# Performance work log

Hardware: AMD Instinct MI355X
Metric: run time of the kernel (lower is better)

The kernel has to match this reference:

```python
import jax, jax.numpy as jnp
import numpy as np

E = 1024
M = 6
GH = 256
FR = 16  # FiLM bottleneck r = max(16, E//64)


def setup_inputs() -> dict:
    key = jax.random.key(0)
    ks = jax.random.split(key, 32)
    n = lambda k, shape, std=0.02: jax.random.normal(k, shape, dtype=jnp.float32) * std
    inp = {
        "x": jax.random.normal(ks[0], (4, 2048, E), dtype=jnp.float32),
        # gate MLP E->GH->M
        "gw1": n(ks[1], (E, GH)), "gb1": jnp.zeros((GH,), jnp.float32),
        "gw2": n(ks[2], (GH, M)), "gb2": jnp.zeros((M,), jnp.float32),
        "ebias": jnp.zeros((M,), jnp.float32),
        "pm_alpha": jnp.float32(0.5),
        # expert 0: DoubleMLP E->2E->E
        "dfc_w": n(ks[3], (E, 2 * E)), "dfc_b": jnp.zeros((2 * E,), jnp.float32),
        "dproj_w": n(ks[4], (2 * E, E)), "dproj_b": jnp.zeros((E,), jnp.float32),
        # expert 1: SingleMLP E->E->E
        "sfc_w": n(ks[5], (E, E)), "sfc_b": jnp.zeros((E,), jnp.float32),
        "sproj_w": n(ks[6], (E, E)), "sproj_b": jnp.zeros((E,), jnp.float32),
        # expert 2: rank-2 perceptron
        "p2_w": n(ks[7], (2, E)), "p2_v": n(ks[8], (2, E)),
        "p2_alpha": jnp.ones((2,), jnp.float32), "p2_b": jnp.zeros((2,), jnp.float32),
        "p2_bias": jnp.zeros((E,), jnp.float32),
        # expert 3: rank-4 perceptron
        "p4_w": n(ks[9], (4, E)), "p4_v": n(ks[10], (4, E)),
        "p4_alpha": jnp.ones((4,), jnp.float32), "p4_b": jnp.zeros((4,), jnp.float32),
        "p4_bias": jnp.zeros((E,), jnp.float32),
        # expert 4: ReGLU1D
        "rg_u": n(ks[11], (E,)), "rg_a": jnp.ones((E,), jnp.float32),
        "rg_b": jnp.zeros((1,), jnp.float32), "rg_bias": jnp.zeros((E,), jnp.float32),
        # expert 5: FiLM E->FR->2E
        "fl_dw": n(ks[12], (E, FR)), "fl_db": jnp.zeros((FR,), jnp.float32),
        "fl_uw": n(ks[13], (FR, 2 * E)), "fl_ub": jnp.zeros((2 * E,), jnp.float32),
    }
    return inp


def _gelu(x):
    return jax.nn.gelu(x, approximate=False)  # torch nn.GELU default (erf)


def _rank_n(x, w, v, alpha, b, biasvec):
    # y = biasvec + sum_i alpha_i * gelu(<w_i,x> + b_i) * v_i
    s = jnp.einsum("bse,ne->bsn", x, w) + b
    g = _gelu(s)
    return jnp.einsum("bsn,ne->bse", alpha * g, v) + biasvec


def reference(x, gw1, gb1, gw2, gb2, ebias, pm_alpha,
              dfc_w, dfc_b, dproj_w, dproj_b,
              sfc_w, sfc_b, sproj_w, sproj_b,
              p2_w, p2_v, p2_alpha, p2_b, p2_bias,
              p4_w, p4_v, p4_alpha, p4_b, p4_bias,
              rg_u, rg_a, rg_b, rg_bias,
              fl_dw, fl_db, fl_uw, fl_ub):
    # gate logits [B,S,M]; tau=1.0
    gl = _gelu(x @ gw1 + gb1) @ gw2 + gb2 + ebias
    pi = jax.nn.softmax(gl, axis=-1)
    # top_k=1 sparse weights: mask to top-1 then renormalize
    _, topi = jax.lax.top_k(pi, 1)
    mask = jax.nn.one_hot(topi[..., 0], M, dtype=pi.dtype)
    w = pi * mask
    w = w / (jnp.sum(w, axis=-1, keepdims=True) + 1e-9)

    # experts (dropout = identity in eval)
    o0 = _gelu(x @ dfc_w + dfc_b) @ dproj_w + dproj_b            # DoubleMLP
    o1 = _gelu(x @ sfc_w + sfc_b) @ sproj_w + sproj_b            # SingleMLP
    o2 = _rank_n(x, p2_w, p2_v, p2_alpha, p2_b, p2_bias)          # perc2
    o3 = _rank_n(x, p4_w, p4_v, p4_alpha, p4_b, p4_bias)          # perc4
    s = x @ rg_u + rg_b[0]                                        # ReGLU1D
    o4 = jax.nn.sigmoid(s)[..., None] * (x * rg_a) + rg_bias
    t = _gelu(x @ fl_dw + fl_db)                                  # FiLM
    gb = t @ fl_uw + fl_ub
    gamma, beta = jnp.split(gb, 2, axis=-1)
    o5 = gamma * x + beta

    all_out = jnp.stack([o0, o1, o2, o3, o4, o5], axis=-1)        # [B,S,E,M]
    mixed = jnp.sum(all_out * w[..., None, :], axis=-1)
    return pm_alpha * mixed
```

## Files before the change

### kernel.cpp

```cpp
#include <hip/hip_runtime.h>
#include <math.h>


#define E 1024
#define GH 256
#define NEXP 6
#define NTOK 8192

typedef __attribute__((ext_vector_type(8))) short bf16x8;
typedef __attribute__((ext_vector_type(4))) float f32x4;

__device__ __forceinline__ float gelu_erf(float v) {
    return 0.5f * v * (1.0f + erff(v * 0.70710678118654752440f));
}

__device__ __forceinline__ unsigned short f2bf(float f) {
    union { float f; unsigned u; } c; c.f = f;
    unsigned u = c.u;
    u += 0x7fffu + ((u >> 16) & 1u);
    return (unsigned short)(u >> 16);
}

__device__ __forceinline__ float bf2f(unsigned short h) {
    union { unsigned u; float f; } c; c.u = ((unsigned)h) << 16;
    return c.f;
}

__device__ __forceinline__ float dot4(float4 a, float4 b) {
    return a.x * b.x + a.y * b.y + a.z * b.z + a.w * b.w;
}

__device__ __forceinline__ int ldso(int row, int q) {
    return row * 32 + ((q ^ ((row >> 1) & 3)) << 3);
}

__global__ __launch_bounds__(256)
void prep_kernel(const float* __restrict__ x, unsigned short* __restrict__ xh,
                 unsigned short* __restrict__ xl,
                 const float* __restrict__ gw1, unsigned short* __restrict__ w1cat,
                 const float* __restrict__ fl_dw, float* __restrict__ fl_dwT,
                 const float* __restrict__ dfc_w, unsigned short* __restrict__ dfc_wt,
                 const float* __restrict__ dproj_w, unsigned short* __restrict__ dpj_wt,
                 const float* __restrict__ sfc_w, unsigned short* __restrict__ sfc_wt,
                 const float* __restrict__ sproj_w, unsigned short* __restrict__ spj_wt) {
    __shared__ float tile[32][33];
    const int tid = threadIdx.x;
    const int tx = tid & 31, ty = tid >> 5;
    int b = blockIdx.x;
    if (b < 2048) {
        const int n4 = NTOK * E / 4;
        for (int i = b * 256 + tid; i < n4; i += 2048 * 256) {
            float4 v = reinterpret_cast<const float4*>(x)[i];
            ushort4 h, l;
            h.x = f2bf(v.x); l.x = f2bf(v.x - bf2f(h.x));
            h.y = f2bf(v.y); l.y = f2bf(v.y - bf2f(h.y));
            h.z = f2bf(v.z); l.z = f2bf(v.z - bf2f(h.z));
            h.w = f2bf(v.w); l.w = f2bf(v.w - bf2f(h.w));
            reinterpret_cast<ushort4*>(xh)[i] = h;
            reinterpret_cast<ushort4*>(xl)[i] = l;
        }
        return;
    }
    b -= 2048;
    if (b < 256) {
        const int c0 = (b & 7) * 32, r0 = (b >> 3) * 32;
#pragma unroll
        for (int i = 0; i < 4; ++i)
            tile[ty + i * 8][tx] = gw1[(size_t)(r0 + ty + i * 8) * GH + c0 + tx];
        __syncthreads();
#pragma unroll
        for (int i = 0; i < 4; ++i) {
            float v = tile[tx][ty + i * 8];
            unsigned short h = f2bf(v);
            size_t row = (size_t)(c0 + ty + i * 8) * 2048;
            w1cat[row + r0 + tx] = h;
            w1cat[row + 1024 + r0 + tx] = f2bf(v - bf2f(h));
        }
        return;
    }
    b -= 256;
    if (b < 64) {
        int idx = b * 256 + tid;
        int j = idx >> 10, k = idx & (E - 1);
        fl_dwT[idx] = fl_dw[k * 16 + j];
        return;
    }
    b -= 64;
    const float* src; unsigned short* dst; int R, C, nbx;
    if (b < 2048)      { src = dfc_w;   dst = dfc_wt; R = 1024; C = 2048; nbx = 64; }
    else if (b < 4096) { src = dproj_w; dst = dpj_wt; R = 2048; C = 1024; nbx = 32; b -= 2048; }
    else if (b < 5120) { src = sfc_w;   dst = sfc_wt; R = 1024; C = 1024; nbx = 32; b -= 4096; }
    else               { src = sproj_w; dst = spj_wt; R = 1024; C = 1024; nbx = 32; b -= 5120; }
    const int c0 = (b % nbx) * 32, r0 = (b / nbx) * 32;
#pragma unroll
    for (int i = 0; i < 4; ++i)
        tile[ty + i * 8][tx] = src[(size_t)(r0 + ty + i * 8) * C + c0 + tx];
    __syncthreads();
#pragma unroll
    for (int i = 0; i < 4; ++i)
        dst[(size_t)(c0 + ty + i * 8) * R + r0 + tx] = f2bf(tile[tx][ty + i * 8]);
}

__global__ __launch_bounds__(256)
void gate_partial_kernel(const unsigned short* __restrict__ xh,
                         const unsigned short* __restrict__ xl,
                         const unsigned short* __restrict__ w1cat,
                         float* __restrict__ hp0, float* __restrict__ hp1) {
    __shared__ __align__(16) unsigned short As[128 * 32];
    __shared__ __align__(16) unsigned short Bs[64 * 32];
    const int tid = threadIdx.x;
    const int t0 = blockIdx.y * 128, n0 = blockIdx.x * 64, z = blockIdx.z;
    const unsigned short* A = z ? xl : xh;
    float* hp = z ? hp1 : hp0;

    const int lane = tid & 63, wv = tid >> 6;
    const int wm = (wv & 1) * 64, wn = (wv >> 1) * 32;
    const int lm = lane & 15, q = lane >> 4;
    const int r0 = tid >> 2, gsl = tid & 3;
    const int g = gsl ^ ((r0 >> 1) & 3);

    const unsigned short* pa0 = A + (size_t)(t0 + r0) * E + g * 8;
    const unsigned short* pa1 = A + (size_t)(t0 + r0 + 64) * E + g * 8;
    const unsigned short* pb0 = w1cat + (size_t)(n0 + r0) * 2048 + g * 8;

    f32x4 acc[4][2];
#pragma unroll
    for (int s = 0; s < 4; ++s)
#pragma unroll
        for (int t = 0; t < 2; ++t) acc[s][t] = (f32x4){0.f, 0.f, 0.f, 0.f};

    bf16x8 ra0 = *(const bf16x8*)(pa0);
    bf16x8 ra1 = *(const bf16x8*)(pa1);
    bf16x8 rb0 = *(const bf16x8*)(pb0);
    *(bf16x8*)&As[r0 * 32 + gsl * 8] = ra0;
    *(bf16x8*)&As[(r0 + 64) * 32 + gsl * 8] = ra1;
    *(bf16x8*)&Bs[r0 * 32 + gsl * 8] = rb0;

    int k0 = 0;
    while (true) {
        __syncthreads();
        const int kn = k0 + 32;
        if (kn < 2048) {
            ra0 = *(const bf16x8*)(pa0 + (kn & 1023));
            ra1 = *(const bf16x8*)(pa1 + (kn & 1023));
            rb0 = *(const bf16x8*)(pb0 + kn);
        }
        bf16x8 af[4], bf[2];
#pragma unroll
        for (int s = 0; s < 4; ++s) af[s] = *(const bf16x8*)&As[ldso(wm + s * 16 + lm, q)];
#pragma unroll
        for (int t = 0; t < 2; ++t) bf[t] = *(const bf16x8*)&Bs[ldso(wn + t * 16 + lm, q)];
#pragma unroll
        for (int s = 0; s < 4; ++s)
#pragma unroll
            for (int t = 0; t < 2; ++t)
                acc[s][t] = __builtin_amdgcn_mfma_f32_16x16x32_bf16(af[s], bf[t], acc[s][t], 0, 0, 0);
        if (kn >= 2048) break;
        __syncthreads();
        *(bf16x8*)&As[r0 * 32 + gsl * 8] = ra0;
        *(bf16x8*)&As[(r0 + 64) * 32 + gsl * 8] = ra1;
        *(bf16x8*)&Bs[r0 * 32 + gsl * 8] = rb0;
        k0 = kn;
    }
#pragma unroll
    for (int s = 0; s < 4; ++s)
#pragma unroll
        for (int t = 0; t < 2; ++t)
#pragma unroll
            for (int rg = 0; rg < 4; ++rg) {
                int rl = wm + s * 16 + q * 4 + rg;
                int c  = wn + t * 16 + lm;
                hp[(size_t)(t0 + rl) * GH + n0 + c] = acc[s][t][rg];
            }
}

__global__ __launch_bounds__(256)
void gate_finalize_kernel(const float* __restrict__ hp0, const float* __restrict__ hp1,
                          const float* __restrict__ gb1, const float* __restrict__ gw2,
                          const float* __restrict__ gb2, const float* __restrict__ ebias,
                          const float* __restrict__ pm_alpha,
                          float* __restrict__ scale, int* __restrict__ counts,
                          int* __restrict__ tlist, int* __restrict__ eid) {
    __shared__ float hs[32][264];
    __shared__ float g2s[GH * NEXP];
    __shared__ int tokexp[32];
    const int tid = threadIdx.x;
    const int t0 = blockIdx.x * 32;
    for (int i = tid; i < GH * NEXP; i += 256) g2s[i] = gw2[i];
#pragma unroll
    for (int i = 0; i < 8; ++i) {
        int f4 = i * 256 + tid;
        int row = f4 >> 6, c4 = (f4 & 63) * 4;
        size_t base = (size_t)(t0 + row) * GH + c4;
        float4 a = *reinterpret_cast<const float4*>(&hp0[base]);
        float4 b = *reinterpret_cast<const float4*>(&hp1[base]);
        float4 o;
        o.x = gelu_erf(a.x + b.x + gb1[c4 + 0]);
        o.y = gelu_erf(a.y + b.y + gb1[c4 + 1]);
        o.z = gelu_erf(a.z + b.z + gb1[c4 + 2]);
        o.w = gelu_erf(a.w + b.w + gb1[c4 + 3]);
        *reinterpret_cast<float4*>(&hs[row][c4]) = o;
    }
    __syncthreads();
    const int t = tid >> 3, j = tid & 7;
    float p[NEXP] = {0.f, 0.f, 0.f, 0.f, 0.f, 0.f};
#pragma unroll 8
    for (int kk = 0; kk < 32; ++kk) {
        int k = j + kk * 8;
        float hv = hs[t][k];
        const float* gr = &g2s[k * NEXP];
#pragma unroll
        for (int m = 0; m < NEXP; ++m) p[m] += hv * gr[m];
    }
#pragma unroll
    for (int m = 0; m < NEXP; ++m) {
        p[m] += __shfl_xor(p[m], 4, 64);
        p[m] += __shfl_xor(p[m], 2, 64);
        p[m] += __shfl_xor(p[m], 1, 64);
    }
    if (j == 0) {
        float L[NEXP];
#pragma unroll
        for (int m = 0; m < NEXP; ++m) L[m] = p[m] + gb2[m] + ebias[m];
        float mx = L[0]; int am = 0;
#pragma unroll
        for (int m = 1; m < NEXP; ++m) { if (L[m] > mx) { mx = L[m]; am = m; } }
        float S = 0.f;
#pragma unroll
        for (int m = 0; m < NEXP; ++m) S += expf(L[m] - mx);
        float pt = 1.f / S;
        scale[t0 + t] = pm_alpha[0] * (pt / (pt + 1e-9f));
        eid[t0 + t] = am;
        tokexp[t] = am;
    }
    __syncthreads();
    if (tid < NEXP) {
        const int e = tid;
        int cnt = 0;
#pragma unroll
        for (int i = 0; i < 32; ++i) cnt += (tokexp[i] == e);
        if (cnt) {
            int base = atomicAdd(&counts[e], cnt);
            int pos = 0;
#pragma unroll
            for (int i = 0; i < 32; ++i)
                if (tokexp[i] == e) tlist[e * NTOK + base + (pos++)] = t0 + i;
        }
    }
}

__global__ __launch_bounds__(256)
void moe_gemm1_kernel(const unsigned short* __restrict__ xh,
                      const unsigned short* __restrict__ B0, const unsigned short* __restrict__ B1,
                      const float* __restrict__ bias0, const float* __restrict__ bias1,
                      const int* __restrict__ counts, const int* __restrict__ tlist,
                      unsigned short* __restrict__ H0, unsigned short* __restrict__ H1) {
    const int z = blockIdx.z;
    const int N = z ? 1024 : 2048;
    const int K = E;
    const int cnt = counts[z];
    const int i0 = blockIdx.y * 64;
    const int n0 = blockIdx.x * 64;
    if (i0 >= cnt || n0 >= N) return;
    const unsigned short* Bz = z ? B1 : B0;
    const float* bias = z ? bias1 : bias0;

    __shared__ __align__(16) unsigned short As[64 * 32];
    __shared__ __align__(16) unsigned short Bs[64 * 32];
    __shared__ int toks[64];
    const int tid = threadIdx.x;
    if (tid < 64) toks[tid] = tlist[z * NTOK + min(i0 + tid, cnt - 1)];
    __syncthreads();

    const int lane = tid & 63, wv = tid >> 6;
    const int wm = (wv & 1) * 32, wn = (wv >> 1) * 32;
    const int lm = lane & 15, q = lane >> 4;
    const int r0 = tid >> 2, gsl = tid & 3;
    const int g = gsl ^ ((r0 >> 1) & 3);

    const unsigned short* pa = xh + (size_t)toks[r0] * K + g * 8;
    const unsigned short* pb = Bz + (size_t)(n0 + r0) * K + g * 8;

    f32x4 acc[2][2];
#pragma unroll
    for (int s = 0; s < 2; ++s)
#pragma unroll
        for (int t = 0; t < 2; ++t) acc[s][t] = (f32x4){0.f, 0.f, 0.f, 0.f};

    bf16x8 ra = *(const bf16x8*)(pa);
    bf16x8 rb = *(const bf16x8*)(pb);
    *(bf16x8*)&As[r0 * 32 + gsl * 8] = ra;
    *(bf16x8*)&Bs[r0 * 32 + gsl * 8] = rb;

    int k0 = 0;
    while (true) {
        __syncthreads();
        const int kn = k0 + 32;
        if (kn < K) {
            ra = *(const bf16x8*)(pa + kn);
            rb = *(const bf16x8*)(pb + kn);
        }
        bf16x8 af[2], bf[2];
#pragma unroll
        for (int s = 0; s < 2; ++s) af[s] = *(const bf16x8*)&As[ldso(wm + s * 16 + lm, q)];
#pragma unroll
        for (int t = 0; t < 2; ++t) bf[t] = *(const bf16x8*)&Bs[ldso(wn + t * 16 + lm, q)];
#pragma unroll
        for (int s = 0; s < 2; ++s)
#pragma unroll
            for (int t = 0; t < 2; ++t)
                acc[s][t] = __builtin_amdgcn_mfma_f32_16x16x32_bf16(af[s], bf[t], acc[s][t], 0, 0, 0);
        if (kn >= K) break;
        __syncthreads();
        *(bf16x8*)&As[r0 * 32 + gsl * 8] = ra;
        *(bf16x8*)&Bs[r0 * 32 + gsl * 8] = rb;
        k0 = kn;
    }
    unsigned short* Hz = z ? H1 : H0;
#pragma unroll
    for (int s = 0; s < 2; ++s)
#pragma unroll
        for (int t = 0; t < 2; ++t)
#pragma unroll
            for (int rg = 0; rg < 4; ++rg) {
                int rl = wm + s * 16 + q * 4 + rg;
                int gc = n0 + wn + t * 16 + lm;
                float v = acc[s][t][rg] + bias[gc];
                Hz[(size_t)(i0 + rl) * N + gc] = f2bf(gelu_erf(v));
            }
}

__global__ __launch_bounds__(256)
void gemm2_cheap_kernel(const unsigned short* __restrict__ h1, const unsigned short* __restrict__ h2,
                        const unsigned short* __restrict__ dpj, const unsigned short* __restrict__ spj,
                        const float* __restrict__ dproj_b, const float* __restrict__ sproj_b,
                        const int* __restrict__ counts, const int* __restrict__ tlist,
                        const float* __restrict__ scale,
                        const float* __restrict__ x, const int* __restrict__ eid,
                        const float* __restrict__ p2_w, const float* __restrict__ p2_v,
                        const float* __restrict__ p2_alpha, const float* __restrict__ p2_b,
                        const float* __restrict__ p2_bias,
                        const float* __restrict__ p4_w, const float* __restrict__ p4_v,
                        const float* __restrict__ p4_alpha, const float* __restrict__ p4_b,
                        const float* __restrict__ p4_bias,
                        const float* __restrict__ rg_u, const float* __restrict__ rg_a,
                        const float* __restrict__ rg_b, const float* __restrict__ rg_bias,
                        const float* __restrict__ fl_dwT, const float* __restrict__ fl_db,
                        const float* __restrict__ fl_uw, const float* __restrict__ fl_ub,
                        float* __restrict__ out) {
    __shared__ __align__(16) char smem[64 * 32 * 2 * 2 + 64 * 4];
    const int tid = threadIdx.x;
    const int bb = blockIdx.x;

    if (bb < 1024) {
        const int z = bb >> 9;
        const int r = bb & 511;
        const int n0 = (r & 15) * 64;
        const int i0 = (r >> 4) * 64;
        const int K = z ? 1024 : 2048;
        const int cnt = counts[z];
        if (i0 >= cnt) return;
        const int rows = min(64, cnt - i0);
        const unsigned short* Az = z ? h2 : h1;
        const unsigned short* Bz = z ? spj : dpj;
        const float* bias = z ? sproj_b : dproj_b;

        unsigned short* As = (unsigned short*)smem;
        unsigned short* Bs = As + 64 * 32;
        int* toks = (int*)(Bs + 64 * 32);
        if (tid < 64) toks[tid] = tlist[z * NTOK + min(i0 + tid, cnt - 1)];
        __syncthreads();

        const int lane = tid & 63, wv = tid >> 6;
        const int wm = (wv & 1) * 32, wn = (wv >> 1) * 32;
        const int lm = lane & 15, q = lane >> 4;
        const int r0 = tid >> 2, gsl = tid & 3;
        const int g = gsl ^ ((r0 >> 1) & 3);

        const unsigned short* pa = Az + (size_t)(i0 + r0) * K + g * 8;
        const unsigned short* pb = Bz + (size_t)(n0 + r0) * K + g * 8;

        f32x4 acc[2][2];
#pragma unroll
        for (int s = 0; s < 2; ++s)
#pragma unroll
            for (int t = 0; t < 2; ++t) acc[s][t] = (f32x4){0.f, 0.f, 0.f, 0.f};

        bf16x8 ra = *(const bf16x8*)(pa);
        bf16x8 rb = *(const bf16x8*)(pb);
        *(bf16x8*)&As[r0 * 32 + gsl * 8] = ra;
        *(bf16x8*)&Bs[r0 * 32 + gsl * 8] = rb;

        int k0 = 0;
        while (true) {
            __syncthreads();
            const int kn = k0 + 32;
            if (kn < K) {
                ra = *(const bf16x8*)(pa + kn);
                rb = *(const bf16x8*)(pb + kn);
            }
            bf16x8 af[2], bf[2];
#pragma unroll
            for (int s = 0; s < 2; ++s) af[s] = *(const bf16x8*)&As[ldso(wm + s * 16 + lm, q)];
#pragma unroll
            for (int t = 0; t < 2; ++t) bf[t] = *(const bf16x8*)&Bs[ldso(wn + t * 16 + lm, q)];
#pragma unroll
            for (int s = 0; s < 2; ++s)
#pragma unroll
                for (int t = 0; t < 2; ++t)
                    acc[s][t] = __builtin_amdgcn_mfma_f32_16x16x32_bf16(af[s], bf[t], acc[s][t], 0, 0, 0);
            if (kn >= K) break;
            __syncthreads();
            *(bf16x8*)&As[r0 * 32 + gsl * 8] = ra;
            *(bf16x8*)&Bs[r0 * 32 + gsl * 8] = rb;
            k0 = kn;
        }
#pragma unroll
        for (int s = 0; s < 2; ++s)
#pragma unroll
            for (int t = 0; t < 2; ++t)
#pragma unroll
                for (int rg = 0; rg < 4; ++rg) {
                    int rl = wm + s * 16 + q * 4 + rg;
                    if (rl < rows) {
                        int gc = n0 + wn + t * 16 + lm;
                        int tok = toks[rl];
                        out[(size_t)tok * E + gc] = scale[tok] * (acc[s][t][rg] + bias[gc]);
                    }
                }
        return;
    }

    const int tok = bb - 1024;
    const int e = eid[tok];
    if (e < 2) return;
    float* red = (float*)smem;
    float* gs  = red + 64;
    const int k4 = tid * 4;
    const float4 xv = *reinterpret_cast<const float4*>(&x[(size_t)tok * E + k4]);
    const float sc = scale[tok];
    const int lane = tid & 63, wid = tid >> 6;
    float4 o;

    if (e == 2 || e == 3) {
        const int n = (e == 2) ? 2 : 4;
        const float* w    = (e == 2) ? p2_w : p4_w;
        const float* v    = (e == 2) ? p2_v : p4_v;
        const float* al   = (e == 2) ? p2_alpha : p4_alpha;
        const float* b    = (e == 2) ? p2_b : p4_b;
        const float* bias = (e == 2) ? p2_bias : p4_bias;
        for (int j = 0; j < n; ++j) {
            float val = dot4(xv, *reinterpret_cast<const float4*>(&w[j * E + k4]));
            for (int off = 32; off > 0; off >>= 1) val += __shfl_down(val, off, 64);
            if (lane == 0) red[j * 4 + wid] = val;
        }
        __syncthreads();
        if (tid < n) {
            float s = red[tid * 4] + red[tid * 4 + 1] + red[tid * 4 + 2] + red[tid * 4 + 3] + b[tid];
            gs[tid] = al[tid] * gelu_erf(s);
        }
        __syncthreads();
        o = *reinterpret_cast<const float4*>(&bias[k4]);
        for (int j = 0; j < n; ++j) {
            float4 vv = *reinterpret_cast<const float4*>(&v[j * E + k4]);
            float gj = gs[j];
            o.x += gj * vv.x; o.y += gj * vv.y; o.z += gj * vv.z; o.w += gj * vv.w;
        }
    } else if (e == 4) {
        float val = dot4(xv, *reinterpret_cast<const float4*>(&rg_u[k4]));
        for (int off = 32; off > 0; off >>= 1) val += __shfl_down(val, off, 64);
        if (lane == 0) red[wid] = val;
        __syncthreads();
        float s = red[0] + red[1] + red[2] + red[3] + rg_b[0];
        float sg = 1.f / (1.f + expf(-s));
        float4 av = *reinterpret_cast<const float4*>(&rg_a[k4]);
        float4 bv = *reinterpret_cast<const float4*>(&rg_bias[k4]);
        o.x = sg * xv.x * av.x + bv.x;
        o.y = sg * xv.y * av.y + bv.y;
        o.z = sg * xv.z * av.z + bv.z;
        o.w = sg * xv.w * av.w + bv.w;
    } else {
#pragma unroll
        for (int j = 0; j < 16; ++j) {
            float val = dot4(xv, *reinterpret_cast<const float4*>(&fl_dwT[j * E + k4]));
            for (int off = 32; off > 0; off >>= 1) val += __shfl_down(val, off, 64);
            if (lane == 0) red[j * 4 + wid] = val;
        }
        __syncthreads();
        if (tid < 16)
            gs[tid] = gelu_erf(red[tid * 4] + red[tid * 4 + 1] + red[tid * 4 + 2] + red[tid * 4 + 3] + fl_db[tid]);
        __syncthreads();
        float4 ga = *reinterpret_cast<const float4*>(&fl_ub[k4]);
        float4 be = *reinterpret_cast<const float4*>(&fl_ub[E + k4]);
#pragma unroll
        for (int j = 0; j < 16; ++j) {
            float tj = gs[j];
            float4 ug = *reinterpret_cast<const float4*>(&fl_uw[(size_t)j * 2 * E + k4]);
            float4 ub = *reinterpret_cast<const float4*>(&fl_uw[(size_t)j * 2 * E + E + k4]);
            ga.x += tj * ug.x; ga.y += tj * ug.y; ga.z += tj * ug.z; ga.w += tj * ug.w;
            be.x += tj * ub.x; be.y += tj * ub.y; be.z += tj * ub.z; be.w += tj * ub.w;
        }
        o.x = ga.x * xv.x + be.x;
        o.y = ga.y * xv.y + be.y;
        o.z = ga.z * xv.z + be.z;
        o.w = ga.w * xv.w + be.w;
    }
    o.x *= sc; o.y *= sc; o.z *= sc; o.w *= sc;
    *reinterpret_cast<float4*>(&out[(size_t)tok * E + k4]) = o;
}

extern "C" void kernel_launch(void* const* d_in, const int* in_sizes, int n_in,
                              void* d_out, int out_size, void* d_ws, size_t ws_size,
                              hipStream_t stream) {
    const float* x        = (const float*)d_in[0];
    const float* gw1      = (const float*)d_in[1];
    const float* gb1      = (const float*)d_in[2];
    const float* gw2      = (const float*)d_in[3];
    const float* gb2      = (const float*)d_in[4];
    const float* ebias    = (const float*)d_in[5];
    const float* pm_alpha = (const float*)d_in[6];
    const float* dfc_w    = (const float*)d_in[7];
    const float* dfc_b    = (const float*)d_in[8];
    const float* dproj_w  = (const float*)d_in[9];
    const float* dproj_b  = (const float*)d_in[10];
    const float* sfc_w    = (const float*)d_in[11];
    const float* sfc_b    = (const float*)d_in[12];
    const float* sproj_w  = (const float*)d_in[13];
    const float* sproj_b  = (const float*)d_in[14];
    const float* p2_w     = (const float*)d_in[15];
    const float* p2_v     = (const float*)d_in[16];
    const float* p2_alpha = (const float*)d_in[17];
    const float* p2_b     = (const float*)d_in[18];
    const float* p2_bias  = (const float*)d_in[19];
    const float* p4_w     = (const float*)d_in[20];
    const float* p4_v     = (const float*)d_in[21];
    const float* p4_alpha = (const float*)d_in[22];
    const float* p4_b     = (const float*)d_in[23];
    const float* p4_bias  = (const float*)d_in[24];
    const float* rg_u     = (const float*)d_in[25];
    const float* rg_a     = (const float*)d_in[26];
    const float* rg_b     = (const float*)d_in[27];
    const float* rg_bias  = (const float*)d_in[28];
    const float* fl_dw    = (const float*)d_in[29];
    const float* fl_db    = (const float*)d_in[30];
    const float* fl_uw    = (const float*)d_in[31];
    const float* fl_ub    = (const float*)d_in[32];
    float* out = (float*)d_out;

    char* ws = (char*)d_ws;
    size_t off = 0;
    int*            counts = (int*)(ws + off);            off += 256;
    float*          scale  = (float*)(ws + off);          off += (size_t)NTOK * 4;
    int*            tlist  = (int*)(ws + off);            off += (size_t)NEXP * NTOK * 4;
    int*            eid    = (int*)(ws + off);            off += (size_t)NTOK * 4;
    float*          fl_dwT = (float*)(ws + off);          off += (size_t)16 * E * 4;
    unsigned short* w1cat  = (unsigned short*)(ws + off); off += (size_t)GH * 2048 * 2;
    unsigned short* dfc_wt = (unsigned short*)(ws + off); off += (size_t)2048 * 1024 * 2;
    unsigned short* dpj_wt = (unsigned short*)(ws + off); off += (size_t)1024 * 2048 * 2;
    unsigned short* sfc_wt = (unsigned short*)(ws + off); off += (size_t)1024 * 1024 * 2;
    unsigned short* spj_wt = (unsigned short*)(ws + off); off += (size_t)1024 * 1024 * 2;
    unsigned short* x_hi   = (unsigned short*)(ws + off); off += (size_t)NTOK * E * 2;
    char* U = ws + off;
    unsigned short* x_lo = (unsigned short*)U;
    float*          hp0  = (float*)(U + (size_t)16 * 1024 * 1024);
    float*          hp1  = (float*)(U + (size_t)24 * 1024 * 1024);
    unsigned short* h1   = (unsigned short*)U;
    unsigned short* h2   = (unsigned short*)(U + (size_t)16 * 1024 * 1024);

    hipMemsetAsync(counts, 0, 256, stream);
    prep_kernel<<<8512, 256, 0, stream>>>(x, x_hi, x_lo, gw1, w1cat, fl_dw, fl_dwT,
                                          dfc_w, dfc_wt, dproj_w, dpj_wt,
                                          sfc_w, sfc_wt, sproj_w, spj_wt);
    gate_partial_kernel<<<dim3(GH / 64, NTOK / 128, 2), 256, 0, stream>>>(x_hi, x_lo, w1cat, hp0, hp1);
    gate_finalize_kernel<<<NTOK / 32, 256, 0, stream>>>(hp0, hp1, gb1, gw2, gb2, ebias,
                                                        pm_alpha, scale, counts, tlist, eid);
    moe_gemm1_kernel<<<dim3(32, 32, 2), 256, 0, stream>>>(
        x_hi, dfc_wt, sfc_wt, dfc_b, sfc_b, counts, tlist, h1, h2);
    gemm2_cheap_kernel<<<1024 + NTOK, 256, 0, stream>>>(
        h1, h2, dpj_wt, spj_wt, dproj_b, sproj_b, counts, tlist, scale,
        x, eid,
        p2_w, p2_v, p2_alpha, p2_b, p2_bias,
        p4_w, p4_v, p4_alpha, p4_b, p4_bias,
        rg_u, rg_a, rg_b, rg_bias,
        fl_dwT, fl_db, fl_uw, fl_ub, out);
    (void)in_sizes; (void)n_in; (void)out_size; (void)ws_size;
}
```

Measured before the change: 297.9 us.

## Double-buffer LDS tiles in all GEMM kernels and shrink gate tile to 64 rows

The three MFMA GEMM loops (gate partial, expert GEMM1, expert GEMM2) now keep two shared-memory buffers for A and B. Each k-step writes the next tile into the idle buffer, which removes one __syncthreads per iteration. The gate partial kernel also moves from 128-row to 64-row token tiles, doubling its grid to give more blocks and less per-block register use. In exchange, LDS usage per block doubles and the gate GEMM reloads weight tiles across twice as many blocks.

```diff
diff --git a/kernel.cpp b/kernel.cpp
--- a/kernel.cpp
+++ b/kernel.cpp
@@ -106,64 +106,59 @@
                          const unsigned short* __restrict__ xl,
                          const unsigned short* __restrict__ w1cat,
                          float* __restrict__ hp0, float* __restrict__ hp1) {
-    __shared__ __align__(16) unsigned short As[128 * 32];
-    __shared__ __align__(16) unsigned short Bs[64 * 32];
+    __shared__ __align__(16) unsigned short As[2][64 * 32];
+    __shared__ __align__(16) unsigned short Bs[2][64 * 32];
     const int tid = threadIdx.x;
-    const int t0 = blockIdx.y * 128, n0 = blockIdx.x * 64, z = blockIdx.z;
+    const int t0 = blockIdx.y * 64, n0 = blockIdx.x * 64, z = blockIdx.z;
     const unsigned short* A = z ? xl : xh;
     float* hp = z ? hp1 : hp0;
 
     const int lane = tid & 63, wv = tid >> 6;
-    const int wm = (wv & 1) * 64, wn = (wv >> 1) * 32;
+    const int wm = (wv & 1) * 32, wn = (wv >> 1) * 32;
     const int lm = lane & 15, q = lane >> 4;
     const int r0 = tid >> 2, gsl = tid & 3;
     const int g = gsl ^ ((r0 >> 1) & 3);
-
-    const unsigned short* pa0 = A + (size_t)(t0 + r0) * E + g * 8;
-    const unsigned short* pa1 = A + (size_t)(t0 + r0 + 64) * E + g * 8;
-    const unsigned short* pb0 = w1cat + (size_t)(n0 + r0) * 2048 + g * 8;
-
-    f32x4 acc[4][2];
-#pragma unroll
-    for (int s = 0; s < 4; ++s)
+    const int so = r0 * 32 + gsl * 8;
+
+    const unsigned short* pa = A + (size_t)(t0 + r0) * E + g * 8;
+    const unsigned short* pb = w1cat + (size_t)(n0 + r0) * 2048 + g * 8;
+
+    f32x4 acc[2][2];
+#pragma unroll
+    for (int s = 0; s < 2; ++s)
 #pragma unroll
         for (int t = 0; t < 2; ++t) acc[s][t] = (f32x4){0.f, 0.f, 0.f, 0.f};
 
-    bf16x8 ra0 = *(const bf16x8*)(pa0);
-    bf16x8 ra1 = *(const bf16x8*)(pa1);
-    bf16x8 rb0 = *(const bf16x8*)(pb0);
-    *(bf16x8*)&As[r0 * 32 + gsl * 8] = ra0;
-    *(bf16x8*)&As[(r0 + 64) * 32 + gsl * 8] = ra1;
-    *(bf16x8*)&Bs[r0 * 32 + gsl * 8] = rb0;
-
-    int k0 = 0;
+    bf16x8 ra = *(const bf16x8*)(pa);
+    bf16x8 rb = *(const bf16x8*)(pb);
+    *(bf16x8*)&As[0][so] = ra;
+    *(bf16x8*)&Bs[0][so] = rb;
+
+    int cur = 0, k0 = 0;
     while (true) {
         __syncthreads();
         const int kn = k0 + 32;
         if (kn < 2048) {
-            ra0 = *(const bf16x8*)(pa0 + (kn & 1023));
-            ra1 = *(const bf16x8*)(pa1 + (kn & 1023));
-            rb0 = *(const bf16x8*)(pb0 + kn);
-        }
-        bf16x8 af[4], bf[2];
-#pragma unroll
-        for (int s = 0; s < 4; ++s) af[s] = *(const bf16x8*)&As[ldso(wm + s * 16 + lm, q)];
-#pragma unroll
-        for (int t = 0; t < 2; ++t) bf[t] = *(const bf16x8*)&Bs[ldso(wn + t * 16 + lm, q)];
-#pragma unroll
-        for (int s = 0; s < 4; ++s)
+            ra = *(const bf16x8*)(pa + (kn & 1023));
+            rb = *(const bf16x8*)(pb + kn);
+        }
+        bf16x8 af[2], bf[2];
+#pragma unroll
+        for (int s = 0; s < 2; ++s) af[s] = *(const bf16x8*)&As[cur][ldso(wm + s * 16 + lm, q)];
+#pragma unroll
+        for (int t = 0; t < 2; ++t) bf[t] = *(const bf16x8*)&Bs[cur][ldso(wn + t * 16 + lm, q)];
+#pragma unroll
+        for (int s = 0; s < 2; ++s)
 #pragma unroll
             for (int t = 0; t < 2; ++t)
                 acc[s][t] = __builtin_amdgcn_mfma_f32_16x16x32_bf16(af[s], bf[t], acc[s][t], 0, 0, 0);
         if (kn >= 2048) break;
-        __syncthreads();
-        *(bf16x8*)&As[r0 * 32 + gsl * 8] = ra0;
-        *(bf16x8*)&As[(r0 + 64) * 32 + gsl * 8] = ra1;
-        *(bf16x8*)&Bs[r0 * 32 + gsl * 8] = rb0;
-        k0 = kn;
-    }
-#pragma unroll
-    for (int s = 0; s < 4; ++s)
+        *(bf16x8*)&As[cur ^ 1][so] = ra;
+        *(bf16x8*)&Bs[cur ^ 1][so] = rb;
+        cur ^= 1; k0 = kn;
+    }
+#pragma unroll
+    for (int s = 0; s < 2; ++s)
 #pragma unroll
         for (int t = 0; t < 2; ++t)
 #pragma unroll
@@ -257,7 +252,6 @@
                       unsigned short* __restrict__ H0, unsigned short* __restrict__ H1) {
     const int z = blockIdx.z;
     const int N = z ? 1024 : 2048;
-    const int K = E;
     const int cnt = counts[z];
     const int i0 = blockIdx.y * 64;
     const int n0 = blockIdx.x * 64;
@@ -265,8 +259,8 @@
     const unsigned short* Bz = z ? B1 : B0;
     const float* bias = z ? bias1 : bias0;
 
-    __shared__ __align__(16) unsigned short As[64 * 32];
-    __shared__ __align__(16) unsigned short Bs[64 * 32];
+    __shared__ __align__(16) unsigned short As[2][64 * 32];
+    __shared__ __align__(16) unsigned short Bs[2][64 * 32];
     __shared__ int toks[64];
     const int tid = threadIdx.x;
     if (tid < 64) toks[tid] = tlist[z * NTOK + min(i0 + tid, cnt - 1)];
@@ -277,9 +271,10 @@
     const int lm = lane & 15, q = lane >> 4;
     const int r0 = tid >> 2, gsl = tid & 3;
     const int g = gsl ^ ((r0 >> 1) & 3);
-
-    const unsigned short* pa = xh + (size_t)toks[r0] * K + g * 8;
-    const unsigned short* pb = Bz + (size_t)(n0 + r0) * K + g * 8;
+    const int so = r0 * 32 + gsl * 8;
+
+    const unsigned short* pa = xh + (size_t)toks[r0] * E + g * 8;
+    const unsigned short* pb = Bz + (size_t)(n0 + r0) * E + g * 8;
 
     f32x4 acc[2][2];
 #pragma unroll
@@ -289,32 +284,31 @@
 
     bf16x8 ra = *(const bf16x8*)(pa);
     bf16x8 rb = *(const bf16x8*)(pb);
-    *(bf16x8*)&As[r0 * 32 + gsl * 8] = ra;
-    *(bf16x8*)&Bs[r0 * 32 + gsl * 8] = rb;
-
-    int k0 = 0;
+    *(bf16x8*)&As[0][so] = ra;
+    *(bf16x8*)&Bs[0][so] = rb;
+
+    int cur = 0, k0 = 0;
     while (true) {
         __syncthreads();
         const int kn = k0 + 32;
-        if (kn < K) {
+        if (kn < E) {
             ra = *(const bf16x8*)(pa + kn);
             rb = *(const bf16x8*)(pb + kn);
         }
         bf16x8 af[2], bf[2];
 #pragma unroll
-        for (int s = 0; s < 2; ++s) af[s] = *(const bf16x8*)&As[ldso(wm + s * 16 + lm, q)];
-#pragma unroll
-        for (int t = 0; t < 2; ++t) bf[t] = *(const bf16x8*)&Bs[ldso(wn + t * 16 + lm, q)];
+        for (int s = 0; s < 2; ++s) af[s] = *(const bf16x8*)&As[cur][ldso(wm + s * 16 + lm, q)];
+#pragma unroll
+        for (int t = 0; t < 2; ++t) bf[t] = *(const bf16x8*)&Bs[cur][ldso(wn + t * 16 + lm, q)];
 #pragma unroll
         for (int s = 0; s < 2; ++s)
 #pragma unroll
             for (int t = 0; t < 2; ++t)
                 acc[s][t] = __builtin_amdgcn_mfma_f32_16x16x32_bf16(af[s], bf[t], acc[s][t], 0, 0, 0);
-        if (kn >= K) break;
-        __syncthreads();
-        *(bf16x8*)&As[r0 * 32 + gsl * 8] = ra;
-        *(bf16x8*)&Bs[r0 * 32 + gsl * 8] = rb;
-        k0 = kn;
+        if (kn >= E) break;
+        *(bf16x8*)&As[cur ^ 1][so] = ra;
+        *(bf16x8*)&Bs[cur ^ 1][so] = rb;
+        cur ^= 1; k0 = kn;
     }
     unsigned short* Hz = z ? H1 : H0;
 #pragma unroll
@@ -348,9 +342,10 @@
                         const float* __restrict__ fl_dwT, const float* __restrict__ fl_db,
                         const float* __restrict__ fl_uw, const float* __restrict__ fl_ub,
                         float* __restrict__ out) {
-    __shared__ __align__(16) char smem[64 * 32 * 2 * 2 + 64 * 4];
+    __shared__ __align__(16) char smem[2 * 64 * 32 * 2 * 2 + 64 * 4];
     const int tid = threadIdx.x;
     const int bb = blockIdx.x;
+    const int lane = tid & 63;
 
     if (bb < 1024) {
         const int z = bb >> 9;
@@ -365,17 +360,18 @@
         const unsigned short* Bz = z ? spj : dpj;
         const float* bias = z ? sproj_b : dproj_b;
 
-        unsigned short* As = (unsigned short*)smem;
-        unsigned short* Bs = As + 64 * 32;
-        int* toks = (int*)(Bs + 64 * 32);
+        unsigned short (*As)[64 * 32] = (unsigned short (*)[64 * 32])smem;
+        unsigned short (*Bs)[64 * 32] = (unsigned short (*)[64 * 32])(smem + 2 * 64 * 32 * 2);
+        int* toks = (int*)(smem + 2 * 64 * 32 * 2 * 2);
         if (tid < 64) toks[tid] = tlist[z * NTOK + min(i0 + tid, cnt - 1)];
         __syncthreads();
 
-        const int lane = tid & 63, wv = tid >> 6;
+        const int wv = tid >> 6;
         const int wm = (wv & 1) * 32, wn = (wv >> 1) * 32;
         const int lm = lane & 15, q = lane >> 4;
         const int r0 = tid >> 2, gsl = tid & 3;
         const int g = gsl ^ ((r0 >> 1) & 3);
+        const int so = r0 * 32 + gsl * 8;
 
         const unsigned short* pa = Az + (size_t)(i0 + r0) * K + g * 8;
         const unsigned short* pb = Bz + (size_t)(n0 + r0) * K + g * 8;
@@ -388,10 +384,10 @@
 
         bf16x8 ra = *(const bf16x8*)(pa);
         bf16x8 rb = *(const bf16x8*)(pb);
-        *(bf16x8*)&As[r0 * 32 + gsl * 8] = ra;
-        *(bf16x8*)&Bs[r0 * 32 + gsl * 8] = rb;
-
-        int k0 = 0;
+        *(bf16x8*)&As[0][so] = ra;
+        *(bf16x8*)&Bs[0][so] = rb;
+
+        int cur = 0, k0 = 0;
         while (true) {
             __syncthreads();
             const int kn = k0 + 32;
@@ -401,19 +397,18 @@
             }
             bf16x8 af[2], bf[2];
 #pragma unroll
-            for (int s = 0; s < 2; ++s) af[s] = *(const bf16x8*)&As[ldso(wm + s * 16 + lm, q)];
-#pragma unroll
-            for (int t = 0; t < 2; ++t) bf[t] = *(const bf16x8*)&Bs[ldso(wn + t * 16 + lm, q)];
+            for (int s = 0; s < 2; ++s) af[s] = *(const bf16x8*)&As[cur][ldso(wm + s * 16 + lm, q)];
+#pragma unroll
+            for (int t = 0; t < 2; ++t) bf[t] = *(const bf16x8*)&Bs[cur][ldso(wn + t * 16 + lm, q)];
 #pragma unroll
             for (int s = 0; s < 2; ++s)
 #pragma unroll
                 for (int t = 0; t < 2; ++t)
                     acc[s][t] = __builtin_amdgcn_mfma_f32_16x16x32_bf16(af[s], bf[t], acc[s][t], 0, 0, 0);
             if (kn >= K) break;
-            __syncthreads();
-            *(bf16x8*)&As[r0 * 32 + gsl * 8] = ra;
-            *(bf16x8*)&Bs[r0 * 32 + gsl * 8] = rb;
-            k0 = kn;
+            *(bf16x8*)&As[cur ^ 1][so] = ra;
+            *(bf16x8*)&Bs[cur ^ 1][so] = rb;
+            cur ^= 1; k0 = kn;
         }
 #pragma unroll
         for (int s = 0; s < 2; ++s)
@@ -439,7 +434,7 @@
     const int k4 = tid * 4;
     const float4 xv = *reinterpret_cast<const float4*>(&x[(size_t)tok * E + k4]);
     const float sc = scale[tok];
-    const int lane = tid & 63, wid = tid >> 6;
+    const int wid = tid >> 6;
     float4 o;
 
     if (e == 2 || e == 3) {
@@ -571,7 +566,7 @@
     prep_kernel<<<8512, 256, 0, stream>>>(x, x_hi, x_lo, gw1, w1cat, fl_dw, fl_dwT,
                                           dfc_w, dfc_wt, dproj_w, dpj_wt,
                                           sfc_w, sfc_wt, sproj_w, spj_wt);
-    gate_partial_kernel<<<dim3(GH / 64, NTOK / 128, 2), 256, 0, stream>>>(x_hi, x_lo, w1cat, hp0, hp1);
+    gate_partial_kernel<<<dim3(GH / 64, NTOK / 64, 2), 256, 0, stream>>>(x_hi, x_lo, w1cat, hp0, hp1);
     gate_finalize_kernel<<<NTOK / 32, 256, 0, stream>>>(hp0, hp1, gb1, gw2, gb2, ebias,
                                                         pm_alpha, scale, counts, tlist, eid);
     moe_gemm1_kernel<<<dim3(32, 32, 2), 256, 0, stream>>>(
```

New measurement: 296.3 us. About the same (-0.5%).
